# Performance work log

Hardware: AMD Instinct MI355X
Metric: run time of the kernel (lower is better)

## Reference

```python
import jax, jax.numpy as jnp
import numpy as np

N_CLASSES = 5
IGNORE_LB = 255
MAX_INDEX = 128          # indexes are drawn in [1, MAX_INDEX]
B, D, H, W = 2, 64, 512, 512
S = N_CLASSES * MAX_INDEX + 1   # static segment capacity: key = max*label + index <= max*n_classes


def setup_inputs() -> dict:
    key = jax.random.key(0)
    k1, k2, k3 = jax.random.split(key, 3)
    feature_out = jax.random.normal(k1, (B, D, H, W), dtype=jnp.float32)
    labels = jax.random.randint(k2, (B, H, W), 0, N_CLASSES).astype(jnp.int64)
    indexes = jax.random.randint(k3, (B, H, W), 1, MAX_INDEX + 1).astype(jnp.int64)
    return {"feature_out": feature_out, "labels": labels, "indexes": indexes}


def _huber(r):
    # torch.where(ret < 1, 0.5*ret**2, ret - 0.5)
    return jnp.where(r < 1.0, 0.5 * r * r, r - 0.5)


def _per_image(feat, label, index):
    # feat: [P, D] float; label, index: [P] int
    m = index.max()                                   # torch: max = index_single.max() (before remap)
    ig = label == IGNORE_LB
    lab = jnp.where(ig, 0, label)
    idx = jnp.where(ig, 0, index)
    keyv = (m * lab + idx).astype(jnp.int32)          # combined sort key; ignore pixels -> key 0

    # Segment mean pooling (replaces sort + nonzero + python cat loop).
    counts = jax.ops.segment_sum(jnp.ones(keyv.shape, jnp.float32), keyv, num_segments=S)
    sums = jax.ops.segment_sum(feat, keyv, num_segments=S)        # [S, D]
    means = sums / jnp.maximum(counts, 1.0)[:, None]

    seg = jnp.arange(S)
    # Original keeps only segments with key != 0 (non-ignore) and size >= 2
    # (the `index_range[i+1]-index_range[i] > 1` style checks).
    valid = (counts >= 2.0) & (seg != 0)
    # class of segment key k: ceil(k/max) - 1  (== label for index in [1, max])
    cls = (jnp.ceil(seg.astype(jnp.float32) / m.astype(jnp.float32)) - 1.0).astype(jnp.int32)
    cmask = ((cls[None, :] == jnp.arange(N_CLASSES)[:, None]) & valid[None, :]).astype(jnp.float32)  # [C, S]

    # Pairwise mean-abs-distance between all segment means: A[i,j] = mean_D |m_i - m_j|
    A = jnp.mean(jnp.abs(means[:, None, :] - means[None, :, :]), axis=-1)  # [S, S]

    pairsum = cmask @ A @ cmask.T                      # [C, C] sum of A over (seg in c1, seg in c2)
    n_c = cmask.sum(-1)                                # segments per class
    npair = n_c[:, None] * n_c[None, :]
    ret = pairsum / jnp.maximum(npair, 1.0)            # torch.mean(|x - y|) per class pair
    h = _huber(ret)

    tri = jnp.triu(jnp.ones((N_CLASSES, N_CLASSES), jnp.float32), k=1)
    pv = tri * (npair > 0.0)                           # unordered pairs of non-empty class groups
    return jnp.sum(h * pv), jnp.sum(pv)


def reference(feature_out, labels, indexes):
    Bn = feature_out.shape[0]
    feat = jnp.transpose(feature_out, (0, 2, 3, 1)).reshape(Bn, -1, feature_out.shape[1])  # [B, P, D]
    lab = labels.reshape(Bn, -1)
    idx = indexes.reshape(Bn, -1)
    s, c = jax.vmap(_per_image)(feat, lab, idx)
    tot_s, tot_c = s.sum(), c.sum()
    mean_h = tot_s / jnp.maximum(tot_c, 1.0)           # torch.mean(torch.stack(losses))
    mean_h = jnp.maximum(mean_h, jnp.float32(1e-12))   # guard log(0)
    Bf = jnp.asarray(Bn, jnp.float32)
    # loss = -mean_h; return -log(-loss/B). If no pairs: loss = -B -> -log(1) = 0.
    out = jnp.where(tot_c > 0.0, -jnp.log(mean_h / Bf), jnp.float32(0.0))
    return out.reshape(1)
```

## Files before the change

### kernel.cpp

```cpp
#include <hip/hip_runtime.h>
#include <math.h>

#define BATCH 2
#define DCH 64
#define PIX (512 * 512)
#define NCLS 5
#define IGNORE_LB 255
#define KSTR 129
#define NSEG 645
#define NBLK 64
#define TI 16

#define OFF_PAIR  0
#define OFF_SUM   256
#define ZERO_BYTES 330496
#define OFF_CNT   330496
#define OFF_BASE  335872
#define OFF_BHIST 341248
#define OFF_KEYS  671488
#define OFF_SKEY  1720064
#define OFF_POS   2768640
#define OFF_FEATS 4865792

__global__ void k_zero(float4* __restrict__ p) {
    const int n4 = ZERO_BYTES / 16;
    for (int i = blockIdx.x * blockDim.x + threadIdx.x; i < n4;
         i += gridDim.x * blockDim.x)
        p[i] = make_float4(0.f, 0.f, 0.f, 0.f);
}

__device__ __forceinline__ unsigned short f2bf(float f) {
    unsigned int u = __float_as_uint(f);
    u += 0x7FFFu + ((u >> 16) & 1u);
    return (unsigned short)(u >> 16);
}

__global__ void k_keys(const int* __restrict__ lab, const int* __restrict__ idx,
                       unsigned short* __restrict__ keys,
                       unsigned int* __restrict__ blockHist) {
    __shared__ unsigned int hist[NSEG];
    const int b = blockIdx.y, blk = blockIdx.x;
    for (int i = threadIdx.x; i < NSEG; i += blockDim.x) hist[i] = 0u;
    __syncthreads();
    const int4* lb = (const int4*)(lab + (size_t)b * PIX);
    const int4* ib = (const int4*)(idx + (size_t)b * PIX);
    unsigned short* kb = keys + (size_t)b * PIX;
    #pragma unroll
    for (int it = 0; it < 4; ++it) {
        const int g = blk * 1024 + it * 256 + threadIdx.x;
        const int4 l4 = lb[g];
        const int4 x4 = ib[g];
        int k[4];
        k[0] = (l4.x == IGNORE_LB) ? 0 : KSTR * l4.x + x4.x;
        k[1] = (l4.y == IGNORE_LB) ? 0 : KSTR * l4.y + x4.y;
        k[2] = (l4.z == IGNORE_LB) ? 0 : KSTR * l4.z + x4.z;
        k[3] = (l4.w == IGNORE_LB) ? 0 : KSTR * l4.w + x4.w;
        ushort4 o;
        o.x = (unsigned short)k[0]; o.y = (unsigned short)k[1];
        o.z = (unsigned short)k[2]; o.w = (unsigned short)k[3];
        *(ushort4*)(kb + 4 * g) = o;
        #pragma unroll
        for (int j = 0; j < 4; ++j) atomicAdd(&hist[k[j]], 1u);
    }
    __syncthreads();
    unsigned int* bh = blockHist + ((size_t)b * NBLK + blk) * NSEG;
    for (int i = threadIdx.x; i < NSEG; i += blockDim.x) bh[i] = hist[i];
}

__global__ void k_scan(unsigned int* __restrict__ blockHist,
                       unsigned int* __restrict__ counts,
                       unsigned int* __restrict__ base) {
    __shared__ unsigned int tot[NSEG];
    const int b = blockIdx.x;
    unsigned int* bh = blockHist + (size_t)b * NBLK * NSEG;
    for (int s = threadIdx.x; s < NSEG; s += blockDim.x) {
        unsigned int run = 0u;
        #pragma unroll 8
        for (int blk = 0; blk < NBLK; ++blk) {
            const unsigned int t = bh[(size_t)blk * NSEG + s];
            bh[(size_t)blk * NSEG + s] = run;
            run += t;
        }
        tot[s] = run;
        counts[b * NSEG + s] = run;
    }
    __syncthreads();
    if (threadIdx.x < 64) {
        const int lane = threadIdx.x;
        unsigned int carry = 0u;
        for (int c = 0; c < (NSEG + 63) / 64; ++c) {
            const int s = c * 64 + lane;
            unsigned int v0 = (s < NSEG) ? tot[s] : 0u;
            unsigned int v = v0;
            #pragma unroll
            for (int o = 1; o < 64; o <<= 1) {
                unsigned int t = __shfl_up(v, o, 64);
                if (lane >= o) v += t;
            }
            if (s < NSEG) base[b * NSEG + s] = carry + (v - v0);
            carry += __shfl(v, 63, 64);
        }
    }
}

__global__ void k_scatter(const unsigned short* __restrict__ keys,
                          const unsigned int* __restrict__ blockHist,
                          const unsigned int* __restrict__ base,
                          unsigned int* __restrict__ posOf,
                          unsigned short* __restrict__ skey) {
    __shared__ unsigned int cur[NSEG];
    const int b = blockIdx.y, blk = blockIdx.x;
    const unsigned int* bh = blockHist + ((size_t)b * NBLK + blk) * NSEG;
    for (int s = threadIdx.x; s < NSEG; s += blockDim.x)
        cur[s] = base[b * NSEG + s] + bh[s];
    __syncthreads();
    const unsigned short* kb = keys + (size_t)b * PIX;
    unsigned int* po = posOf + (size_t)b * PIX;
    unsigned short* sk = skey + (size_t)b * PIX;
    #pragma unroll
    for (int it = 0; it < 4; ++it) {
        const int g = blk * 1024 + it * 256 + threadIdx.x;
        const ushort4 k4 = *(const ushort4*)(kb + 4 * g);
        const unsigned short kk[4] = {k4.x, k4.y, k4.z, k4.w};
        #pragma unroll
        for (int j = 0; j < 4; ++j) {
            const unsigned int pos = atomicAdd(&cur[kk[j]], 1u);
            po[4 * g + j] = pos;
            sk[pos] = kk[j];
        }
    }
}

__global__ __launch_bounds__(256) void k_tpose(const float* __restrict__ feat,
                                               const unsigned int* __restrict__ posOf,
                                               unsigned short* __restrict__ featS) {
    __shared__ unsigned short tile[64][72];
    __shared__ unsigned int posLDS[64];
    const int b = blockIdx.y;
    const int P0 = blockIdx.x * 64;
    const int tid = threadIdx.x;
    if (tid < 64) posLDS[tid] = posOf[(size_t)b * PIX + P0 + tid];
    const float* fb = feat + (size_t)b * DCH * PIX;
    #pragma unroll
    for (int i = 0; i < 4; ++i) {
        const int idx = i * 256 + tid;
        const int ch = idx >> 4, px4 = idx & 15;
        const float4 v = *(const float4*)(fb + (size_t)ch * PIX + P0 + 4 * px4);
        const int col = ch ^ ((px4 & 7) << 3);
        tile[4 * px4 + 0][col] = f2bf(v.x);
        tile[4 * px4 + 1][col] = f2bf(v.y);
        tile[4 * px4 + 2][col] = f2bf(v.z);
        tile[4 * px4 + 3][col] = f2bf(v.w);
    }
    __syncthreads();
    unsigned short* fS = featS + (size_t)b * PIX * DCH;
    #pragma unroll
    for (int i = 0; i < 4; ++i) {
        const int idx = i * 256 + tid;
        const int px = idx >> 4, c4 = idx & 15;
        const int col0 = (4 * c4) ^ (((px >> 2) & 7) << 3);
        const uint2 w = *(const uint2*)&tile[px][col0];
        *(uint2*)(fS + ((size_t)posLDS[px]) * DCH + 4 * c4) = w;
    }
}

__global__ __launch_bounds__(256) void k_segsum(const unsigned short* __restrict__ featS,
                                                const unsigned short* __restrict__ skey,
                                                float* __restrict__ sums) {
    const int b = blockIdx.y;
    const int lane = threadIdx.x & 63, wid = threadIdx.x >> 6;
    const int q0 = (blockIdx.x * 4 + wid) * 64;
    const unsigned short* fS = featS + (size_t)b * PIX * DCH;
    const int sk = skey[(size_t)b * PIX + q0 + lane];
    int cur = __shfl(sk, 0, 64);
    float acc = 0.f;
    #pragma unroll 8
    for (int j = 0; j < 64; ++j) {
        const int k = __shfl(sk, j, 64);
        const unsigned int u = fS[(size_t)(q0 + j) * DCH + lane];
        const float f = __uint_as_float(u << 16);
        if (k != cur) {
            unsafeAtomicAdd(&sums[((size_t)b * NSEG + cur) * DCH + lane], acc);
            acc = 0.f;
            cur = k;
        }
        acc += f;
    }
    unsafeAtomicAdd(&sums[((size_t)b * NSEG + cur) * DCH + lane], acc);
}

__global__ void k_pairs(const float* __restrict__ sums,
                        const unsigned int* __restrict__ counts,
                        float* __restrict__ pairsum) {
    __shared__ float rI[TI][DCH + 1], rJ[TI][DCH + 1];
    __shared__ int cI[TI], cJ[TI];
    __shared__ float ps[NCLS * NCLS];
    const int b = blockIdx.z;
    const int i0 = blockIdx.x * TI, j0 = blockIdx.y * TI;
    if (threadIdx.x < NCLS * NCLS) ps[threadIdx.x] = 0.f;
    for (int t = threadIdx.x; t < TI * DCH; t += blockDim.x) {
        const int r = t >> 6, d = t & 63;
        const int si = i0 + r, sj = j0 + r;
        float vi = 0.f, vj = 0.f;
        if (si < NSEG) {
            const float c = fmaxf((float)counts[b * NSEG + si], 1.f);
            vi = sums[((size_t)b * NSEG + si) * DCH + d] / c;
        }
        if (sj < NSEG) {
            const float c = fmaxf((float)counts[b * NSEG + sj], 1.f);
            vj = sums[((size_t)b * NSEG + sj) * DCH + d] / c;
        }
        rI[r][d] = vi;
        rJ[r][d] = vj;
    }
    if (threadIdx.x < TI) {
        int si = i0 + threadIdx.x;
        bool ok = (si > 0 && si < NSEG && counts[b * NSEG + si] >= 2u);
        cI[threadIdx.x] = ok ? (si - 1) / KSTR : -1;
        int sj = j0 + threadIdx.x;
        ok = (sj > 0 && sj < NSEG && counts[b * NSEG + sj] >= 2u);
        cJ[threadIdx.x] = ok ? (sj - 1) / KSTR : -1;
    }
    __syncthreads();
    const int ti = threadIdx.x >> 4, tj = threadIdx.x & 15;
    const int ci = cI[ti], cj = cJ[tj];
    if (ci >= 0 && ci < NCLS && cj >= 0 && cj < NCLS) {
        float s = 0.f;
        #pragma unroll
        for (int d = 0; d < DCH; ++d) s += fabsf(rI[ti][d] - rJ[tj][d]);
        unsafeAtomicAdd(&ps[ci * NCLS + cj], s * (1.f / DCH));
    }
    __syncthreads();
    if (threadIdx.x < NCLS * NCLS && ps[threadIdx.x] != 0.f)
        unsafeAtomicAdd(&pairsum[b * NCLS * NCLS + threadIdx.x], ps[threadIdx.x]);
}

__global__ void k_final(const unsigned int* __restrict__ counts,
                        const float* __restrict__ pairsum,
                        float* __restrict__ out) {
    __shared__ int nc[BATCH][NCLS];
    __shared__ float psl[BATCH * NCLS * NCLS];
    const int tid = threadIdx.x;
    if (tid < BATCH * NCLS) nc[tid / NCLS][tid % NCLS] = 0;
    if (tid < BATCH * NCLS * NCLS) psl[tid] = pairsum[tid];
    __syncthreads();
    for (int t = tid; t < BATCH * NSEG; t += blockDim.x) {
        const int b = t / NSEG, s = t % NSEG;
        if (s > 0 && counts[t] >= 2u) {
            const int c = (s - 1) / KSTR;
            if (c >= 0 && c < NCLS) atomicAdd(&nc[b][c], 1);
        }
    }
    __syncthreads();
    if (tid == 0) {
        float tot_s = 0.f, tot_c = 0.f;
        for (int b = 0; b < BATCH; ++b)
            for (int c1 = 0; c1 < NCLS; ++c1)
                for (int c2 = c1 + 1; c2 < NCLS; ++c2) {
                    const float np = (float)nc[b][c1] * (float)nc[b][c2];
                    if (np > 0.f) {
                        const float r = psl[b * NCLS * NCLS + c1 * NCLS + c2] / np;
                        tot_s += (r < 1.f) ? 0.5f * r * r : r - 0.5f;
                        tot_c += 1.f;
                    }
                }
        float mh = tot_s / fmaxf(tot_c, 1.f);
        mh = fmaxf(mh, 1e-12f);
        out[0] = (tot_c > 0.f) ? -logf(mh / (float)BATCH) : 0.f;
    }
}

extern "C" void kernel_launch(void* const* d_in, const int* in_sizes, int n_in,
                              void* d_out, int out_size, void* d_ws, size_t ws_size,
                              hipStream_t stream) {
    const float* feat = (const float*)d_in[0];
    const int* lab = (const int*)d_in[1];
    const int* idx = (const int*)d_in[2];
    float* out = (float*)d_out;
    char* ws = (char*)d_ws;

    float* pairsum        = (float*)(ws + OFF_PAIR);
    float* sums           = (float*)(ws + OFF_SUM);
    unsigned int* counts  = (unsigned int*)(ws + OFF_CNT);
    unsigned int* base    = (unsigned int*)(ws + OFF_BASE);
    unsigned int* bhist   = (unsigned int*)(ws + OFF_BHIST);
    unsigned short* keys  = (unsigned short*)(ws + OFF_KEYS);
    unsigned short* skey  = (unsigned short*)(ws + OFF_SKEY);
    unsigned int* posOf   = (unsigned int*)(ws + OFF_POS);
    unsigned short* featS = (unsigned short*)(ws + OFF_FEATS);

    k_zero<<<81, 256, 0, stream>>>((float4*)ws);
    k_keys<<<dim3(NBLK, BATCH), 256, 0, stream>>>(lab, idx, keys, bhist);
    k_scan<<<BATCH, 256, 0, stream>>>(bhist, counts, base);
    k_scatter<<<dim3(NBLK, BATCH), 256, 0, stream>>>(keys, bhist, base, posOf, skey);
    k_tpose<<<dim3(PIX / 64, BATCH), 256, 0, stream>>>(feat, posOf, featS);
    k_segsum<<<dim3(PIX / 256, BATCH), 256, 0, stream>>>(featS, skey, sums);
    k_pairs<<<dim3((NSEG + TI - 1) / TI, (NSEG + TI - 1) / TI, BATCH), 256, 0, stream>>>(
        sums, counts, pairsum);
    k_final<<<1, 256, 0, stream>>>(counts, pairsum, out);
}
```

Measured before the change: 114.5 us.

## Parallelize histogram scan, fuse workspace zeroing, skip lower-triangle pair tiles

```diff
diff --git a/kernel.cpp b/kernel.cpp
--- a/kernel.cpp
+++ b/kernel.cpp
@@ -22,13 +22,6 @@
 #define OFF_POS   2768640
 #define OFF_FEATS 4865792
 
-__global__ void k_zero(float4* __restrict__ p) {
-    const int n4 = ZERO_BYTES / 16;
-    for (int i = blockIdx.x * blockDim.x + threadIdx.x; i < n4;
-         i += gridDim.x * blockDim.x)
-        p[i] = make_float4(0.f, 0.f, 0.f, 0.f);
-}
-
 __device__ __forceinline__ unsigned short f2bf(float f) {
     unsigned int u = __float_as_uint(f);
     u += 0x7FFFu + ((u >> 16) & 1u);
@@ -37,9 +30,19 @@
 
 __global__ void k_keys(const int* __restrict__ lab, const int* __restrict__ idx,
                        unsigned short* __restrict__ keys,
-                       unsigned int* __restrict__ blockHist) {
+                       unsigned int* __restrict__ blockHist,
+                       float4* __restrict__ zeroReg) {
     __shared__ unsigned int hist[NSEG];
     const int b = blockIdx.y, blk = blockIdx.x;
+    {
+        const int n4 = ZERO_BYTES / 16;
+        const int bid = b * NBLK + blk;
+        const int per = (n4 + NBLK * BATCH - 1) / (NBLK * BATCH);
+        const int lo = bid * per;
+        const int hi = (lo + per < n4) ? lo + per : n4;
+        for (int i = lo + threadIdx.x; i < hi; i += blockDim.x)
+            zeroReg[i] = make_float4(0.f, 0.f, 0.f, 0.f);
+    }
     for (int i = threadIdx.x; i < NSEG; i += blockDim.x) hist[i] = 0u;
     __syncthreads();
     const int4* lb = (const int4*)(lab + (size_t)b * PIX);
@@ -67,39 +70,39 @@
     for (int i = threadIdx.x; i < NSEG; i += blockDim.x) bh[i] = hist[i];
 }
 
-__global__ void k_scan(unsigned int* __restrict__ blockHist,
-                       unsigned int* __restrict__ counts,
-                       unsigned int* __restrict__ base) {
-    __shared__ unsigned int tot[NSEG];
-    const int b = blockIdx.x;
-    unsigned int* bh = blockHist + (size_t)b * NBLK * NSEG;
-    for (int s = threadIdx.x; s < NSEG; s += blockDim.x) {
-        unsigned int run = 0u;
-        #pragma unroll 8
-        for (int blk = 0; blk < NBLK; ++blk) {
-            const unsigned int t = bh[(size_t)blk * NSEG + s];
-            bh[(size_t)blk * NSEG + s] = run;
-            run += t;
-        }
-        tot[s] = run;
-        counts[b * NSEG + s] = run;
-    }
-    __syncthreads();
-    if (threadIdx.x < 64) {
-        const int lane = threadIdx.x;
-        unsigned int carry = 0u;
-        for (int c = 0; c < (NSEG + 63) / 64; ++c) {
-            const int s = c * 64 + lane;
-            unsigned int v0 = (s < NSEG) ? tot[s] : 0u;
-            unsigned int v = v0;
-            #pragma unroll
-            for (int o = 1; o < 64; o <<= 1) {
-                unsigned int t = __shfl_up(v, o, 64);
-                if (lane >= o) v += t;
-            }
-            if (s < NSEG) base[b * NSEG + s] = carry + (v - v0);
-            carry += __shfl(v, 63, 64);
-        }
+__global__ void k_scanA(unsigned int* __restrict__ blockHist,
+                        unsigned int* __restrict__ counts) {
+    const int b = blockIdx.y;
+    const int s = blockIdx.x * 4 + (threadIdx.x >> 6);
+    const int lane = threadIdx.x & 63;
+    if (s >= NSEG) return;
+    unsigned int* col = blockHist + (size_t)b * NBLK * NSEG + s;
+    const unsigned int v0 = col[(size_t)lane * NSEG];
+    unsigned int v = v0;
+    #pragma unroll
+    for (int o = 1; o < 64; o <<= 1) {
+        unsigned int t = __shfl_up(v, o, 64);
+        if (lane >= o) v += t;
+    }
+    col[(size_t)lane * NSEG] = v - v0;
+    if (lane == 63) counts[b * NSEG + s] = v;
+}
+
+__global__ void k_scanB(const unsigned int* __restrict__ counts,
+                        unsigned int* __restrict__ base) {
+    const int b = blockIdx.x, lane = threadIdx.x;
+    unsigned int carry = 0u;
+    for (int c = 0; c < (NSEG + 63) / 64; ++c) {
+        const int s = c * 64 + lane;
+        unsigned int v0 = (s < NSEG) ? counts[b * NSEG + s] : 0u;
+        unsigned int v = v0;
+        #pragma unroll
+        for (int o = 1; o < 64; o <<= 1) {
+            unsigned int t = __shfl_up(v, o, 64);
+            if (lane >= o) v += t;
+        }
+        if (s < NSEG) base[b * NSEG + s] = carry + (v - v0);
+        carry += __shfl(v, 63, 64);
     }
 }
 
@@ -192,6 +195,7 @@
 __global__ void k_pairs(const float* __restrict__ sums,
                         const unsigned int* __restrict__ counts,
                         float* __restrict__ pairsum) {
+    if (blockIdx.y < blockIdx.x) return;
     __shared__ float rI[TI][DCH + 1], rJ[TI][DCH + 1];
     __shared__ int cI[TI], cJ[TI];
     __shared__ float ps[NCLS * NCLS];
@@ -289,9 +293,9 @@
     unsigned int* posOf   = (unsigned int*)(ws + OFF_POS);
     unsigned short* featS = (unsigned short*)(ws + OFF_FEATS);
 
-    k_zero<<<81, 256, 0, stream>>>((float4*)ws);
-    k_keys<<<dim3(NBLK, BATCH), 256, 0, stream>>>(lab, idx, keys, bhist);
-    k_scan<<<BATCH, 256, 0, stream>>>(bhist, counts, base);
+    k_keys<<<dim3(NBLK, BATCH), 256, 0, stream>>>(lab, idx, keys, bhist, (float4*)ws);
+    k_scanA<<<dim3((NSEG + 3) / 4, BATCH), 256, 0, stream>>>(bhist, counts);
+    k_scanB<<<BATCH, 64, 0, stream>>>(counts, base);
     k_scatter<<<dim3(NBLK, BATCH), 256, 0, stream>>>(keys, bhist, base, posOf, skey);
     k_tpose<<<dim3(PIX / 64, BATCH), 256, 0, stream>>>(feat, posOf, featS);
     k_segsum<<<dim3(PIX / 256, BATCH), 256, 0, stream>>>(featS, skey, sums);
```

New measurement: 96.38 us. -15.8%, faster.
